# Performance work log

Hardware: AMD Instinct MI355X
Metric: run time of the kernel (lower is better)

## Reference

```python
import jax, jax.numpy as jnp
import numpy as np

N = 100000      # nodes
E = 1600000     # edges
F_IN = 27       # node features
EMB = 64        # embedding size
H = 128         # hidden/out channels
L = 4           # GNN layers
G = 512         # num_graphs


def setup_inputs() -> dict:
    key = jax.random.key(0)
    ks = jax.random.split(key, 13)
    s = 0.05
    return {
        "x": jax.random.normal(ks[0], (N, F_IN), jnp.float32),
        "edge_index": jax.random.randint(ks[1], (2, E), 0, N),
        "batch": jnp.sort(jax.random.randint(ks[2], (N,), 0, G)),
        "lin0_w": jax.random.normal(ks[3], (F_IN, EMB), jnp.float32) * s,
        "ggc_weight": jax.random.normal(ks[4], (L, H, H), jnp.float32) * s,
        "gru_w_ih": jax.random.normal(ks[5], (3 * H, H), jnp.float32) * s,
        "gru_w_hh": jax.random.normal(ks[6], (3 * H, H), jnp.float32) * s,
        "gru_b_ih": jax.random.normal(ks[7], (3 * H,), jnp.float32) * s,
        "gru_b_hh": jax.random.normal(ks[8], (3 * H,), jnp.float32) * s,
        "lin1_w": jax.random.normal(ks[9], (H, 1), jnp.float32) * s,
        "lin1_b": jax.random.normal(ks[10], (1,), jnp.float32) * s,
        "lin2_w": jax.random.normal(ks[11], (H, 1), jnp.float32) * s,
        "lin2_b": jax.random.normal(ks[12], (1,), jnp.float32) * s,
    }


def _gru_cell(m, h, w_ih, w_hh, b_ih, b_hh):
    # torch.nn.GRUCell math
    gi = m @ w_ih.T + b_ih          # [N, 3H]
    gh = h @ w_hh.T + b_hh          # [N, 3H]
    i_r, i_z, i_n = jnp.split(gi, 3, axis=1)
    h_r, h_z, h_n = jnp.split(gh, 3, axis=1)
    r = jax.nn.sigmoid(i_r + h_r)
    z = jax.nn.sigmoid(i_z + h_z)
    n = jnp.tanh(i_n + r * h_n)
    return (1.0 - z) * n + z * h


def reference(x, edge_index, batch, lin0_w, ggc_weight,
              gru_w_ih, gru_w_hh, gru_b_ih, gru_b_hh,
              lin1_w, lin1_b, lin2_w, lin2_b):
    x1 = jax.nn.sigmoid(x @ lin0_w)                       # [N, EMB]
    h = jnp.pad(x1, ((0, 0), (0, H - EMB)))               # pad to out_channels
    src, dst = edge_index[0], edge_index[1]
    for i in range(L):
        m = h @ ggc_weight[i]                             # [N, H]
        m = jax.ops.segment_sum(m[src], dst, num_segments=N)  # add-aggregate at target
        h = _gru_cell(m, h, gru_w_ih, gru_w_hh, gru_b_ih, gru_b_hh)
    xr = jax.nn.relu(h)
    mu = xr @ lin1_w + lin1_b                             # [N, 1]
    sigma = jax.nn.softplus(xr @ lin2_w + lin2_b)         # [N, 1]
    uncorrected_mu = mu
    mu_all = jax.ops.segment_sum(mu, batch, num_segments=G)        # [G, 1]
    sigma_all = jax.ops.segment_sum(sigma, batch, num_segments=G)  # [G, 1]
    # vectorized per-graph correction (original loops over graphs)
    mu_c = mu - mu_all[batch] * (sigma / sigma_all[batch])
    return (mu_c.squeeze(1), x1, sigma.squeeze(1), uncorrected_mu.squeeze(1))
```

## Files before the change

kernel.cpp:

```cpp
#include <hip/hip_runtime.h>
#include <math.h>

#define NN 100000
#define FIN 27
#define EMB 64
#define HH 128
#define LAYERS 4
#define GG 512
#define SCAN_CHUNK 2048
#define SPAN 512
#define SPANSHIFT 9
#define MAXNB 256
#define ECAP 16384
#define LPAD_US 136
#define TM 32

typedef __attribute__((ext_vector_type(8))) short short8;
typedef __attribute__((ext_vector_type(4))) float floatx4;

__device__ __forceinline__ float sigmf(float x) { return 1.0f / (1.0f + __expf(-x)); }
__device__ __forceinline__ float tanhfast(float x) { return 1.0f - 2.0f / (__expf(2.0f * x) + 1.0f); }

__device__ __forceinline__ unsigned short f2bf(float f) {
    unsigned int u = __float_as_uint(f);
    u += 0x7FFFu + ((u >> 16) & 1u);
    return (unsigned short)(u >> 16);
}

__device__ __forceinline__ float bflo(unsigned int v) { return __uint_as_float(v << 16); }
__device__ __forceinline__ float bfhi(unsigned int v) { return __uint_as_float(v & 0xFFFF0000u); }
__device__ __forceinline__ float bfs(unsigned short v) { return __uint_as_float(((unsigned)v) << 16); }

__global__ void lin0_kernel(const float* __restrict__ x, const float* __restrict__ w,
                            float* __restrict__ x1_out, unsigned short* __restrict__ hbf, int n) {
    int wave = (int)((blockIdx.x * blockDim.x + threadIdx.x) >> 6);
    int lane = threadIdx.x & 63;
    if (wave >= n) return;
    const float* xr = x + (size_t)wave * FIN;
    float acc = 0.0f;
#pragma unroll
    for (int k = 0; k < FIN; ++k) acc += xr[k] * w[k * EMB + lane];
    float v = 1.0f / (1.0f + expf(-acc));
    x1_out[(size_t)wave * EMB + lane] = v;
    hbf[(size_t)wave * HH + lane] = f2bf(v);
}

__global__ void bucket_scatter_direct(const int* __restrict__ src, const int* __restrict__ dst,
                                      int* __restrict__ bucket_cnt, unsigned* __restrict__ ebuf,
                                      int e) {
    __shared__ int lh[MAXNB];
    __shared__ int gb[MAXNB];
    int t = threadIdx.x;
    for (int i = t; i < MAXNB; i += 1024) lh[i] = 0;
    __syncthreads();
    int base = blockIdx.x * 16384;
    int lidx[16], sv[16], dv[16];
#pragma unroll
    for (int i = 0; i < 16; ++i) {
        int eid = base + i * 1024 + t;
        if (eid < e) {
            sv[i] = src[eid];
            dv[i] = dst[eid];
            lidx[i] = atomicAdd(&lh[dv[i] >> SPANSHIFT], 1);
        } else lidx[i] = -1;
    }
    __syncthreads();
    for (int i = t; i < MAXNB; i += 1024) {
        int c = lh[i];
        gb[i] = c ? atomicAdd(&bucket_cnt[i], c) : 0;
    }
    __syncthreads();
#pragma unroll
    for (int i = 0; i < 16; ++i) {
        if (lidx[i] >= 0) {
            int b = dv[i] >> SPANSHIFT;
            int pos = gb[b] + lidx[i];
            if (pos < ECAP) {
                unsigned dl = (unsigned)(dv[i] - (b << SPANSHIFT));
                ebuf[(size_t)b * ECAP + pos] = (dl << 17) | (unsigned)sv[i];
            }
        }
    }
}

__global__ void deg_from_buckets(const unsigned* __restrict__ ebuf, const int* __restrict__ bucket_cnt,
                                 int* __restrict__ deg, int n) {
    __shared__ int ld[SPAN];
    int b = blockIdx.x, t = threadIdx.x;
    ld[t] = 0; ld[t + 256] = 0;
    __syncthreads();
    int cnt = bucket_cnt[b];
    if (cnt > ECAP) cnt = ECAP;
    size_t base = (size_t)b * ECAP;
    int nodebase = b << SPANSHIFT;
    for (int j = t; j < cnt; j += 256)
        atomicAdd(&ld[ebuf[base + j] >> 17], 1);
    __syncthreads();
    int i0 = nodebase + t, i1 = nodebase + 256 + t;
    if (i0 < n) deg[i0] = ld[t];
    if (i1 < n) deg[i1] = ld[t + 256];
}

__global__ void scan_partial(const int* __restrict__ deg, int* __restrict__ blocksum, int n) {
    int b = blockIdx.x, t = threadIdx.x;
    int base = b * SCAN_CHUNK + t * 8;
    int s = 0;
#pragma unroll
    for (int i = 0; i < 8; ++i) {
        int idx = base + i;
        if (idx < n) s += deg[idx];
    }
#pragma unroll
    for (int off = 32; off > 0; off >>= 1) s += __shfl_down(s, off, 64);
    __shared__ int ws[4];
    if ((t & 63) == 0) ws[t >> 6] = s;
    __syncthreads();
    if (t == 0) blocksum[b] = ws[0] + ws[1] + ws[2] + ws[3];
}

__global__ void scan_blocksums(const int* __restrict__ blocksum, int* __restrict__ blockoff, int nb) {
    int t = threadIdx.x;
    int own = (t < nb) ? blocksum[t] : 0;
    int v = own;
    for (int off = 1; off < 64; off <<= 1) {
        int u = __shfl_up(v, off, 64);
        if (t >= off) v += u;
    }
    if (t < nb) blockoff[t] = v - own;
}

__global__ void scan_final(const int* __restrict__ deg, const int* __restrict__ blockoff,
                           int* __restrict__ rowptr, int n) {
    int b = blockIdx.x, t = threadIdx.x;
    int base = b * SCAN_CHUNK + t * 8;
    int v[8];
    int s = 0;
#pragma unroll
    for (int i = 0; i < 8; ++i) {
        int idx = base + i;
        v[i] = (idx < n) ? deg[idx] : 0;
        s += v[i];
    }
    __shared__ int ts[256];
    ts[t] = s;
    __syncthreads();
    for (int off = 1; off < 256; off <<= 1) {
        int u = (t >= off) ? ts[t - off] : 0;
        __syncthreads();
        ts[t] += u;
        __syncthreads();
    }
    int run = blockoff[b] + ((t == 0) ? 0 : ts[t - 1]);
#pragma unroll
    for (int i = 0; i < 8; ++i) {
        int idx = base + i;
        if (idx < n) {
            rowptr[idx] = run;
            run += v[i];
        } else if (idx == n) {
            rowptr[n] = run;
        }
    }
}

__global__ void place_kernel(const unsigned* __restrict__ ebuf, const int* __restrict__ bucket_cnt,
                             const int* __restrict__ rowptr, int* __restrict__ col, int n) {
    __shared__ int cur[SPAN];
    int b = blockIdx.x, t = threadIdx.x;
    int nodebase = b << SPANSHIFT;
    int i0 = nodebase + t, i1 = nodebase + 256 + t;
    cur[t] = (i0 < n) ? rowptr[i0] : 0;
    cur[t + 256] = (i1 < n) ? rowptr[i1] : 0;
    __syncthreads();
    int cnt = bucket_cnt[b];
    if (cnt > ECAP) cnt = ECAP;
    size_t base = (size_t)b * ECAP;
    for (int j = t; j < cnt; j += 256) {
        unsigned ed = ebuf[base + j];
        int pos = atomicAdd(&cur[ed >> 17], 1);
        col[pos] = (int)(ed & 0x1FFFFu);
    }
}

__global__ void sort_rows_kernel(const int* __restrict__ rowptr, int* __restrict__ col, int n) {
    int node = (int)((blockIdx.x * blockDim.x + threadIdx.x) >> 6);
    int lane = threadIdx.x & 63;
    if (node >= n) return;
    int r0 = rowptr[node], r1 = rowptr[node + 1];
    int d = r1 - r0;
    if (d <= 1 || d > 64) return;
    int v = (lane < d) ? col[r0 + lane] : 0x7FFFFFFF;
#pragma unroll
    for (int k = 2; k <= 64; k <<= 1) {
#pragma unroll
        for (int j = k >> 1; j > 0; j >>= 1) {
            int u = __shfl_xor(v, j, 64);
            bool dir = (lane & k) == 0;
            bool lower = (lane & j) == 0;
            int mn = min(v, u), mx = max(v, u);
            v = (dir == lower) ? mn : mx;
        }
    }
    if (lane < d) col[r0 + lane] = v;
}

template <int HALF>
__global__ __launch_bounds__(512, 8)
void agg_kernel(const unsigned short* __restrict__ hin, unsigned short* __restrict__ aggout,
                const int* __restrict__ rowptr, const int* __restrict__ col, int n) {
    int node = (int)((blockIdx.x * blockDim.x + threadIdx.x) >> 6);
    int lane = threadIdx.x & 63;
    if (node >= n) return;
    int l16 = lane & 15;
    int lg = lane >> 4;
    const uint4* hin4 = (const uint4*)hin;
    const uint2* hin2 = (const uint2*)hin;
    int r0 = rowptr[node];
    int r1 = rowptr[node + 1];

    if (HALF) {
        float a[4], b[4];
#pragma unroll
        for (int k = 0; k < 4; ++k) { a[k] = 0.0f; b[k] = 0.0f; }
        int j = r0 + lg;
        for (; j + 4 < r1; j += 8) {
            int s0 = col[j], s1 = col[j + 4];
            uint2 v0 = hin2[(size_t)s0 * 32 + l16];
            uint2 v1 = hin2[(size_t)s1 * 32 + l16];
            a[0] += bflo(v0.x); a[1] += bfhi(v0.x);
            a[2] += bflo(v0.y); a[3] += bfhi(v0.y);
            b[0] += bflo(v1.x); b[1] += bfhi(v1.x);
            b[2] += bflo(v1.y); b[3] += bfhi(v1.y);
        }
        for (; j < r1; j += 4) {
            int s = col[j];
            uint2 v = hin2[(size_t)s * 32 + l16];
            a[0] += bflo(v.x); a[1] += bfhi(v.x);
            a[2] += bflo(v.y); a[3] += bfhi(v.y);
        }
#pragma unroll
        for (int k = 0; k < 4; ++k) {
            a[k] += b[k];
            a[k] += __shfl_xor(a[k], 32, 64);
            a[k] += __shfl_xor(a[k], 16, 64);
        }
        if (lg == 0) {
            uint2 o;
            o.x = (unsigned)f2bf(a[0]) | ((unsigned)f2bf(a[1]) << 16);
            o.y = (unsigned)f2bf(a[2]) | ((unsigned)f2bf(a[3]) << 16);
            *(uint2*)(aggout + (size_t)node * HH + l16 * 4) = o;
        }
    } else {
        float a[8], b[8];
#pragma unroll
        for (int k = 0; k < 8; ++k) { a[k] = 0.0f; b[k] = 0.0f; }
        int j = r0 + lg;
        for (; j + 12 < r1; j += 16) {
            int s0 = col[j], s1 = col[j + 4], s2 = col[j + 8], s3 = col[j + 12];
            uint4 v0 = hin4[(size_t)s0 * 16 + l16];
            uint4 v1 = hin4[(size_t)s1 * 16 + l16];
            uint4 v2 = hin4[(size_t)s2 * 16 + l16];
            uint4 v3 = hin4[(size_t)s3 * 16 + l16];
            a[0] += bflo(v0.x); a[1] += bfhi(v0.x);
            a[2] += bflo(v0.y); a[3] += bfhi(v0.y);
            a[4] += bflo(v0.z); a[5] += bfhi(v0.z);
            a[6] += bflo(v0.w); a[7] += bfhi(v0.w);
            b[0] += bflo(v1.x); b[1] += bfhi(v1.x);
            b[2] += bflo(v1.y); b[3] += bfhi(v1.y);
            b[4] += bflo(v1.z); b[5] += bfhi(v1.z);
            b[6] += bflo(v1.w); b[7] += bfhi(v1.w);
            a[0] += bflo(v2.x); a[1] += bfhi(v2.x);
            a[2] += bflo(v2.y); a[3] += bfhi(v2.y);
            a[4] += bflo(v2.z); a[5] += bfhi(v2.z);
            a[6] += bflo(v2.w); a[7] += bfhi(v2.w);
            b[0] += bflo(v3.x); b[1] += bfhi(v3.x);
            b[2] += bflo(v3.y); b[3] += bfhi(v3.y);
            b[4] += bflo(v3.z); b[5] += bfhi(v3.z);
            b[6] += bflo(v3.w); b[7] += bfhi(v3.w);
        }
        for (; j + 4 < r1; j += 8) {
            int s0 = col[j], s1 = col[j + 4];
            uint4 v0 = hin4[(size_t)s0 * 16 + l16];
            uint4 v1 = hin4[(size_t)s1 * 16 + l16];
            a[0] += bflo(v0.x); a[1] += bfhi(v0.x);
            a[2] += bflo(v0.y); a[3] += bfhi(v0.y);
            a[4] += bflo(v0.z); a[5] += bfhi(v0.z);
            a[6] += bflo(v0.w); a[7] += bfhi(v0.w);
            b[0] += bflo(v1.x); b[1] += bfhi(v1.x);
            b[2] += bflo(v1.y); b[3] += bfhi(v1.y);
            b[4] += bflo(v1.z); b[5] += bfhi(v1.z);
            b[6] += bflo(v1.w); b[7] += bfhi(v1.w);
        }
        for (; j < r1; j += 4) {
            int s = col[j];
            uint4 v = hin4[(size_t)s * 16 + l16];
            a[0] += bflo(v.x); a[1] += bfhi(v.x);
            a[2] += bflo(v.y); a[3] += bfhi(v.y);
            a[4] += bflo(v.z); a[5] += bfhi(v.z);
            a[6] += bflo(v.w); a[7] += bfhi(v.w);
        }
#pragma unroll
        for (int k = 0; k < 8; ++k) {
            a[k] += b[k];
            a[k] += __shfl_xor(a[k], 32, 64);
            a[k] += __shfl_xor(a[k], 16, 64);
        }
        if (lg == 0) {
            uint4 o;
            o.x = (unsigned)f2bf(a[0]) | ((unsigned)f2bf(a[1]) << 16);
            o.y = (unsigned)f2bf(a[2]) | ((unsigned)f2bf(a[3]) << 16);
            o.z = (unsigned)f2bf(a[4]) | ((unsigned)f2bf(a[5]) << 16);
            o.w = (unsigned)f2bf(a[6]) | ((unsigned)f2bf(a[7]) << 16);
            *(uint4*)(aggout + (size_t)node * HH + l16 * 8) = o;
        }
    }
}

template <int HALF>
__global__ __launch_bounds__(512, 4)
void gru_kernel(const unsigned short* __restrict__ aggin,
                const unsigned short* __restrict__ hin,
                unsigned short* __restrict__ hout,
                const unsigned short* __restrict__ Wfp,
                const unsigned short* __restrict__ whhp,
                const float* __restrict__ b_ih, const float* __restrict__ b_hh,
                int n) {
    __shared__ unsigned short aggL[TM * LPAD_US];
    __shared__ unsigned short hL[TM * LPAD_US];
    int wave = threadIdx.x >> 6;
    int lane = threadIdx.x & 63;
    int quad = lane >> 4;
    int l15 = lane & 15;
    int M0 = blockIdx.x * TM;
    if (M0 >= n) return;

    {
        int row = threadIdx.x >> 4;
        int q = threadIdx.x & 15;
        int gr = M0 + row;
        uint4 va = make_uint4(0, 0, 0, 0), vh = va;
        if (gr < n && !(HALF && q >= 8)) {
            va = ((const uint4*)aggin)[(size_t)gr * 16 + q];
            vh = ((const uint4*)hin)[(size_t)gr * 16 + q];
        }
        *(uint4*)(&aggL[row * LPAD_US + q * 8]) = va;
        *(uint4*)(&hL[row * LPAD_US + q * 8]) = vh;
    }
    __syncthreads();

    floatx4 gi[2][3], gh[2][3];
#pragma unroll
    for (int m = 0; m < 2; ++m)
#pragma unroll
        for (int g = 0; g < 3; ++g) {
            gi[m][g] = (floatx4)0.0f;
            gh[m][g] = (floatx4)0.0f;
        }

    const int KTMAX = HALF ? 2 : 4;
#pragma unroll
    for (int kt = 0; kt < KTMAX; ++kt) {
        int kbase = kt * 32 + quad * 8;
        short8 aA0 = *(const short8*)(&aggL[l15 * LPAD_US + kbase]);
        short8 aH0 = *(const short8*)(&hL[l15 * LPAD_US + kbase]);
        short8 aA1 = *(const short8*)(&aggL[(16 + l15) * LPAD_US + kbase]);
        short8 aH1 = *(const short8*)(&hL[(16 + l15) * LPAD_US + kbase]);
#pragma unroll
        for (int g = 0; g < 3; ++g) {
            int ct = g * 8 + wave;
            size_t boff = ((size_t)(kt * 24 + ct) * 64 + lane) * 8;
            short8 bi = *(const short8*)(Wfp + boff);
            short8 bh = *(const short8*)(whhp + boff);
            gi[0][g] = __builtin_amdgcn_mfma_f32_16x16x32_bf16(aA0, bi, gi[0][g], 0, 0, 0);
            gi[1][g] = __builtin_amdgcn_mfma_f32_16x16x32_bf16(aA1, bi, gi[1][g], 0, 0, 0);
            gh[0][g] = __builtin_amdgcn_mfma_f32_16x16x32_bf16(aH0, bh, gh[0][g], 0, 0, 0);
            gh[1][g] = __builtin_amdgcn_mfma_f32_16x16x32_bf16(aH1, bh, gh[1][g], 0, 0, 0);
        }
    }

    __syncthreads();

    {
        int c = wave * 16 + l15;
        float bir = b_ih[c], biz = b_ih[128 + c], bin_ = b_ih[256 + c];
        float bhr = b_hh[c], bhz = b_hh[128 + c], bhn = b_hh[256 + c];
#pragma unroll
        for (int m = 0; m < 2; ++m) {
#pragma unroll
            for (int j = 0; j < 4; ++j) {
                int row = m * 16 + quad * 4 + j;
                int lidx = row * LPAD_US + c;
                float gir = gi[m][0][j] + bir;
                float ghr = gh[m][0][j] + bhr;
                float giz = gi[m][1][j] + biz;
                float ghz = gh[m][1][j] + bhz;
                float gin = gi[m][2][j] + bin_;
                float ghn = gh[m][2][j] + bhn;
                float rr = sigmf(gir + ghr);
                float zz = sigmf(giz + ghz);
                float nn = tanhfast(gin + rr * ghn);
                float hp = bfs(hL[lidx]);
                aggL[lidx] = f2bf((1.0f - zz) * nn + zz * hp);
            }
        }
    }

    __syncthreads();

    {
        int row = threadIdx.x >> 4;
        int q = threadIdx.x & 15;
        int gr = M0 + row;
        if (gr < n) {
            uint4 v = *(const uint4*)(&aggL[row * LPAD_US + q * 8]);
            *(uint4*)(hout + (size_t)gr * HH + q * 8) = v;
        }
    }
}

__global__ void pack_whh(const float* __restrict__ w_hh, unsigned short* __restrict__ whhp) {
    int id = blockIdx.x * blockDim.x + threadIdx.x;
    if (id >= 4 * 24 * 64 * 8) return;
    int j = id & 7;
    int lane = (id >> 3) & 63;
    int ctkt = id >> 9;
    int ct = ctkt % 24;
    int kt = ctkt / 24;
    int k = kt * 32 + (lane >> 4) * 8 + j;
    int col = ct * 16 + (lane & 15);
    whhp[id] = f2bf(w_hh[col * HH + k]);
}

__global__ void pack_wf(const float* __restrict__ ggc, const float* __restrict__ w_ih,
                        unsigned short* __restrict__ Wfp) {
    int id = blockIdx.x * blockDim.x + threadIdx.x;
    if (id >= LAYERS * 4 * 24 * 64 * 8) return;
    int l = id / 49152;
    int rem = id % 49152;
    int j = rem & 7;
    int lane = (rem >> 3) & 63;
    int ctkt = rem >> 9;
    int ct = ctkt % 24;
    int kt = ctkt / 24;
    int k = kt * 32 + (lane >> 4) * 8 + j;
    int col = ct * 16 + (lane & 15);
    const float4* gr = (const float4*)(ggc + ((size_t)l * HH + k) * HH);
    const float4* wr = (const float4*)(w_ih + (size_t)col * HH);
    float acc = 0.0f;
#pragma unroll 4
    for (int q = 0; q < HH / 4; ++q) {
        float4 g = gr[q], w = wr[q];
        acc += g.x * w.x + g.y * w.y + g.z * w.z + g.w * w.w;
    }
    Wfp[id] = f2bf(acc);
}

__global__ void readout_kernel(const unsigned int* __restrict__ h2, const float* __restrict__ w1,
                               const float* __restrict__ b1, const float* __restrict__ w2,
                               const float* __restrict__ b2,
                               float* __restrict__ out_mu, float* __restrict__ out_sg, int n) {
    int wave = (int)((blockIdx.x * blockDim.x + threadIdx.x) >> 6);
    int lane = threadIdx.x & 63;
    if (wave >= n) return;
    unsigned int u = h2[(size_t)wave * 64 + lane];
    float x0 = fmaxf(bflo(u), 0.0f);
    float x1 = fmaxf(bfhi(u), 0.0f);
    float2 wv1 = ((const float2*)w1)[lane];
    float2 wv2 = ((const float2*)w2)[lane];
    float a1 = x0 * wv1.x + x1 * wv1.y;
    float a2 = x0 * wv2.x + x1 * wv2.y;
#pragma unroll
    for (int off = 32; off > 0; off >>= 1) {
        a1 += __shfl_down(a1, off, 64);
        a2 += __shfl_down(a2, off, 64);
    }
    if (lane == 0) {
        float mu = a1 + b1[0];
        float x2 = a2 + b2[0];
        float sg = (x2 > 20.0f) ? x2 : __logf(1.0f + __expf(x2));
        out_mu[wave] = mu;
        out_sg[wave] = sg;
    }
}

__device__ __forceinline__ int lbound(const int* __restrict__ a, int n, int v) {
    int lo = 0, hi = n;
    while (lo < hi) {
        int m = (lo + hi) >> 1;
        if (a[m] < v) lo = m + 1; else hi = m;
    }
    return lo;
}

__global__ void seg_correct_kernel(const float* __restrict__ out_mu, const float* __restrict__ out_sg,
                                   const int* __restrict__ batch, float* __restrict__ out_muc, int n) {
    int g = blockIdx.x;
    int lo = lbound(batch, n, g);
    int hi = lbound(batch, n, g + 1);
    float smu = 0.0f, ssg = 0.0f;
    for (int i = lo + threadIdx.x; i < hi; i += blockDim.x) {
        smu += out_mu[i];
        ssg += out_sg[i];
    }
#pragma unroll
    for (int off = 32; off > 0; off >>= 1) {
        smu += __shfl_down(smu, off, 64);
        ssg += __shfl_down(ssg, off, 64);
    }
    __shared__ float pm[4], ps[4];
    int wave = threadIdx.x >> 6;
    int lane = threadIdx.x & 63;
    if (lane == 0) { pm[wave] = smu; ps[wave] = ssg; }
    __syncthreads();
    float tot_mu = pm[0] + pm[1] + pm[2] + pm[3];
    float tot_sg = ps[0] + ps[1] + ps[2] + ps[3];
    for (int i = lo + threadIdx.x; i < hi; i += blockDim.x) {
        out_muc[i] = out_mu[i] - tot_mu * (out_sg[i] / tot_sg);
    }
}

extern "C" void kernel_launch(void* const* d_in, const int* in_sizes, int n_in,
                              void* d_out, int out_size, void* d_ws, size_t ws_size,
                              hipStream_t stream) {
    const float* x      = (const float*)d_in[0];
    const int*   ei     = (const int*)d_in[1];
    const int*   batch  = (const int*)d_in[2];
    const float* lin0_w = (const float*)d_in[3];
    const float* ggc    = (const float*)d_in[4];
    const float* w_ih   = (const float*)d_in[5];
    const float* w_hh   = (const float*)d_in[6];
    const float* b_ih   = (const float*)d_in[7];
    const float* b_hh   = (const float*)d_in[8];
    const float* l1w    = (const float*)d_in[9];
    const float* l1b    = (const float*)d_in[10];
    const float* l2w    = (const float*)d_in[11];
    const float* l2b    = (const float*)d_in[12];

    int n = in_sizes[0] / FIN;
    int e = in_sizes[1] / 2;
    const int* src = ei;
    const int* dstp = ei + e;

    float* out = (float*)d_out;
    float* out_muc = out;
    float* out_x1  = out + n;
    float* out_sg  = out + n + (size_t)n * EMB;
    float* out_mu  = out_sg + n;

    unsigned short* hbf0 = (unsigned short*)d_ws;
    unsigned short* hbf1 = hbf0 + (size_t)n * HH;
    unsigned short* Wfp  = hbf1 + (size_t)n * HH;
    unsigned short* whhp = Wfp + (size_t)LAYERS * 49152;
    int*            deg      = (int*)(whhp + 49152 + 8);
    int*            rowptr   = deg + n;
    int*            blocksum = rowptr + n + 1;
    int*            blockoff = blocksum + 64;
    int*            bucket_cnt = blockoff + 64;
    int*            col      = bucket_cnt + MAXNB;
    unsigned*       ebuf     = (unsigned*)hbf1;

    int nbuck = (n + SPAN - 1) >> SPANSHIFT;
    hipMemsetAsync(bucket_cnt, 0, MAXNB * sizeof(int), stream);

    int wave_blocks = (n * 64 + 255) / 256;
    lin0_kernel<<<wave_blocks, 256, 0, stream>>>(x, lin0_w, out_x1, hbf0, n);

    int eb = (e + 16383) / 16384;
    bucket_scatter_direct<<<eb, 1024, 0, stream>>>(src, dstp, bucket_cnt, ebuf, e);
    deg_from_buckets<<<nbuck, 256, 0, stream>>>(ebuf, bucket_cnt, deg, n);

    int nb = (n + SCAN_CHUNK) / SCAN_CHUNK;
    scan_partial<<<nb, 256, 0, stream>>>(deg, blocksum, n);
    scan_blocksums<<<1, 64, 0, stream>>>(blocksum, blockoff, nb);
    scan_final<<<nb, 256, 0, stream>>>(deg, blockoff, rowptr, n);

    place_kernel<<<nbuck, 256, 0, stream>>>(ebuf, bucket_cnt, rowptr, col, n);

    int node_wave_blocks = (n + 7) / 8;
    sort_rows_kernel<<<node_wave_blocks, 512, 0, stream>>>(rowptr, col, n);

    pack_whh<<<(49152 + 255) / 256, 256, 0, stream>>>(w_hh, whhp);
    pack_wf<<<(LAYERS * 49152 + 255) / 256, 256, 0, stream>>>(ggc, w_ih, Wfp);

    int gru_blocks = (n + TM - 1) / TM;
    unsigned short* hin = hbf0;
    unsigned short* hother = hbf1;
    for (int l = 0; l < LAYERS; ++l) {
        if (l == 0) {
            agg_kernel<1><<<node_wave_blocks, 512, 0, stream>>>(hin, hother, rowptr, col, n);
            gru_kernel<1><<<gru_blocks, 512, 0, stream>>>(hother, hin, hother,
                                                          Wfp, whhp, b_ih, b_hh, n);
        } else {
            agg_kernel<0><<<node_wave_blocks, 512, 0, stream>>>(hin, hother, rowptr, col, n);
            gru_kernel<0><<<gru_blocks, 512, 0, stream>>>(hother, hin, hother,
                                                          Wfp + (size_t)l * 49152, whhp,
                                                          b_ih, b_hh, n);
        }
        unsigned short* t = hin; hin = hother; hother = t;
    }

    readout_kernel<<<wave_blocks, 256, 0, stream>>>((const unsigned int*)hin, l1w, l1b, l2w, l2b,
                                                    out_mu, out_sg, n);
    seg_correct_kernel<<<GG, 256, 0, stream>>>(out_mu, out_sg, batch, out_muc, n);
}
```

Before: 653.8 us.

## Double GRU row tile to 64 and drop per-row neighbor sort kernel

The GRU kernel now processes 64 rows per block instead of 32, so each weight fragment loaded from global memory feeds four MFMA row tiles instead of two. Launch bounds are relaxed to allow more registers for the larger accumulator set. Separately, the bitonic sort of each node's neighbor list is removed, saving a kernel launch, though the order of summation in aggregation then depends on atomic placement and is no longer deterministic. The larger tile raises register and LDS use, which lowers occupancy.

Measured after the change: 667.6 us. 2.1% more time.

```diff
diff --git a/kernel.cpp b/kernel.cpp
--- a/kernel.cpp
+++ b/kernel.cpp
@@ -13,7 +13,7 @@
 #define MAXNB 256
 #define ECAP 16384
 #define LPAD_US 136
-#define TM 32
+#define TM 64
 
 typedef __attribute__((ext_vector_type(8))) short short8;
 typedef __attribute__((ext_vector_type(4))) float floatx4;
@@ -180,28 +180,6 @@
         int pos = atomicAdd(&cur[ed >> 17], 1);
         col[pos] = (int)(ed & 0x1FFFFu);
     }
-}
-
-__global__ void sort_rows_kernel(const int* __restrict__ rowptr, int* __restrict__ col, int n) {
-    int node = (int)((blockIdx.x * blockDim.x + threadIdx.x) >> 6);
-    int lane = threadIdx.x & 63;
-    if (node >= n) return;
-    int r0 = rowptr[node], r1 = rowptr[node + 1];
-    int d = r1 - r0;
-    if (d <= 1 || d > 64) return;
-    int v = (lane < d) ? col[r0 + lane] : 0x7FFFFFFF;
-#pragma unroll
-    for (int k = 2; k <= 64; k <<= 1) {
-#pragma unroll
-        for (int j = k >> 1; j > 0; j >>= 1) {
-            int u = __shfl_xor(v, j, 64);
-            bool dir = (lane & k) == 0;
-            bool lower = (lane & j) == 0;
-            int mn = min(v, u), mx = max(v, u);
-            v = (dir == lower) ? mn : mx;
-        }
-    }
-    if (lane < d) col[r0 + lane] = v;
 }
 
 template <int HALF>
@@ -317,7 +295,7 @@
 }
 
 template <int HALF>
-__global__ __launch_bounds__(512, 4)
+__global__ __launch_bounds__(512, 2)
 void gru_kernel(const unsigned short* __restrict__ aggin,
                 const unsigned short* __restrict__ hin,
                 unsigned short* __restrict__ hout,
@@ -334,9 +312,11 @@
     int M0 = blockIdx.x * TM;
     if (M0 >= n) return;
 
-    {
-        int row = threadIdx.x >> 4;
-        int q = threadIdx.x & 15;
+#pragma unroll
+    for (int i = 0; i < 2; ++i) {
+        int idx = threadIdx.x + i * 512;
+        int row = idx >> 4;
+        int q = idx & 15;
         int gr = M0 + row;
         uint4 va = make_uint4(0, 0, 0, 0), vh = va;
         if (gr < n && !(HALF && q >= 8)) {
@@ -348,9 +328,9 @@
     }
     __syncthreads();
 
-    floatx4 gi[2][3], gh[2][3];
-#pragma unroll
-    for (int m = 0; m < 2; ++m)
+    floatx4 gi[4][3], gh[4][3];
+#pragma unroll
+    for (int m = 0; m < 4; ++m)
 #pragma unroll
         for (int g = 0; g < 3; ++g) {
             gi[m][g] = (floatx4)0.0f;
@@ -361,20 +341,23 @@
 #pragma unroll
     for (int kt = 0; kt < KTMAX; ++kt) {
         int kbase = kt * 32 + quad * 8;
-        short8 aA0 = *(const short8*)(&aggL[l15 * LPAD_US + kbase]);
-        short8 aH0 = *(const short8*)(&hL[l15 * LPAD_US + kbase]);
-        short8 aA1 = *(const short8*)(&aggL[(16 + l15) * LPAD_US + kbase]);
-        short8 aH1 = *(const short8*)(&hL[(16 + l15) * LPAD_US + kbase]);
+        short8 aA[4], aH[4];
+#pragma unroll
+        for (int m = 0; m < 4; ++m) {
+            aA[m] = *(const short8*)(&aggL[(m * 16 + l15) * LPAD_US + kbase]);
+            aH[m] = *(const short8*)(&hL[(m * 16 + l15) * LPAD_US + kbase]);
+        }
 #pragma unroll
         for (int g = 0; g < 3; ++g) {
             int ct = g * 8 + wave;
             size_t boff = ((size_t)(kt * 24 + ct) * 64 + lane) * 8;
             short8 bi = *(const short8*)(Wfp + boff);
             short8 bh = *(const short8*)(whhp + boff);
-            gi[0][g] = __builtin_amdgcn_mfma_f32_16x16x32_bf16(aA0, bi, gi[0][g], 0, 0, 0);
-            gi[1][g] = __builtin_amdgcn_mfma_f32_16x16x32_bf16(aA1, bi, gi[1][g], 0, 0, 0);
-            gh[0][g] = __builtin_amdgcn_mfma_f32_16x16x32_bf16(aH0, bh, gh[0][g], 0, 0, 0);
-            gh[1][g] = __builtin_amdgcn_mfma_f32_16x16x32_bf16(aH1, bh, gh[1][g], 0, 0, 0);
+#pragma unroll
+            for (int m = 0; m < 4; ++m) {
+                gi[m][g] = __builtin_amdgcn_mfma_f32_16x16x32_bf16(aA[m], bi, gi[m][g], 0, 0, 0);
+                gh[m][g] = __builtin_amdgcn_mfma_f32_16x16x32_bf16(aH[m], bh, gh[m][g], 0, 0, 0);
+            }
         }
     }
 
@@ -385,7 +368,7 @@
         float bir = b_ih[c], biz = b_ih[128 + c], bin_ = b_ih[256 + c];
         float bhr = b_hh[c], bhz = b_hh[128 + c], bhn = b_hh[256 + c];
 #pragma unroll
-        for (int m = 0; m < 2; ++m) {
+        for (int m = 0; m < 4; ++m) {
 #pragma unroll
             for (int j = 0; j < 4; ++j) {
                 int row = m * 16 + quad * 4 + j;
@@ -407,9 +390,11 @@
 
     __syncthreads();
 
-    {
-        int row = threadIdx.x >> 4;
-        int q = threadIdx.x & 15;
+#pragma unroll
+    for (int i = 0; i < 2; ++i) {
+        int idx = threadIdx.x + i * 512;
+        int row = idx >> 4;
+        int q = idx & 15;
         int gr = M0 + row;
         if (gr < n) {
             uint4 v = *(const uint4*)(&aggL[row * LPAD_US + q * 8]);
@@ -576,12 +561,10 @@
 
     place_kernel<<<nbuck, 256, 0, stream>>>(ebuf, bucket_cnt, rowptr, col, n);
 
-    int node_wave_blocks = (n + 7) / 8;
-    sort_rows_kernel<<<node_wave_blocks, 512, 0, stream>>>(rowptr, col, n);
-
     pack_whh<<<(49152 + 255) / 256, 256, 0, stream>>>(w_hh, whhp);
     pack_wf<<<(LAYERS * 49152 + 255) / 256, 256, 0, stream>>>(ggc, w_ih, Wfp);
 
+    int node_wave_blocks = (n + 7) / 8;
     int gru_blocks = (n + TM - 1) / TM;
     unsigned short* hin = hbf0;
     unsigned short* hother = hbf1;
```

## Merge aggregation and GRU into chunked launches and drop row sorting

Applied to the files above, without the earlier changes.

Each layer is split into node chunks. One launch runs the GRU update for chunk k-1 alongside the neighbor aggregation for chunk k, so the gather and matrix phases overlap instead of being separated by kernel boundaries. The per-row column sort kernel is removed, which saves a pass but leaves gather order within rows unsorted and may hurt locality. The change adds more launches per layer and a mixed-role block dispatch that can unbalance occupancy.

New measurement: 808.4 us. 1.24x slower.

```diff
diff --git a/kernel.cpp b/kernel.cpp
--- a/kernel.cpp
+++ b/kernel.cpp
@@ -13,7 +13,8 @@
 #define MAXNB 256
 #define ECAP 16384
 #define LPAD_US 136
-#define TM 32
+#define TMG 32
+#define KCH 4
 
 typedef __attribute__((ext_vector_type(8))) short short8;
 typedef __attribute__((ext_vector_type(4))) float floatx4;
@@ -182,238 +183,212 @@
     }
 }
 
-__global__ void sort_rows_kernel(const int* __restrict__ rowptr, int* __restrict__ col, int n) {
-    int node = (int)((blockIdx.x * blockDim.x + threadIdx.x) >> 6);
-    int lane = threadIdx.x & 63;
-    if (node >= n) return;
-    int r0 = rowptr[node], r1 = rowptr[node + 1];
-    int d = r1 - r0;
-    if (d <= 1 || d > 64) return;
-    int v = (lane < d) ? col[r0 + lane] : 0x7FFFFFFF;
-#pragma unroll
-    for (int k = 2; k <= 64; k <<= 1) {
-#pragma unroll
-        for (int j = k >> 1; j > 0; j >>= 1) {
-            int u = __shfl_xor(v, j, 64);
-            bool dir = (lane & k) == 0;
-            bool lower = (lane & j) == 0;
-            int mn = min(v, u), mx = max(v, u);
-            v = (dir == lower) ? mn : mx;
-        }
-    }
-    if (lane < d) col[r0 + lane] = v;
-}
-
-template <int HALF>
-__global__ __launch_bounds__(512, 8)
-void agg_kernel(const unsigned short* __restrict__ hin, unsigned short* __restrict__ aggout,
-                const int* __restrict__ rowptr, const int* __restrict__ col, int n) {
-    int node = (int)((blockIdx.x * blockDim.x + threadIdx.x) >> 6);
-    int lane = threadIdx.x & 63;
-    if (node >= n) return;
-    int l16 = lane & 15;
-    int lg = lane >> 4;
-    const uint4* hin4 = (const uint4*)hin;
-    const uint2* hin2 = (const uint2*)hin;
-    int r0 = rowptr[node];
-    int r1 = rowptr[node + 1];
-
-    if (HALF) {
-        float a[4], b[4];
-#pragma unroll
-        for (int k = 0; k < 4; ++k) { a[k] = 0.0f; b[k] = 0.0f; }
-        int j = r0 + lg;
-        for (; j + 4 < r1; j += 8) {
-            int s0 = col[j], s1 = col[j + 4];
-            uint2 v0 = hin2[(size_t)s0 * 32 + l16];
-            uint2 v1 = hin2[(size_t)s1 * 32 + l16];
-            a[0] += bflo(v0.x); a[1] += bfhi(v0.x);
-            a[2] += bflo(v0.y); a[3] += bfhi(v0.y);
-            b[0] += bflo(v1.x); b[1] += bfhi(v1.x);
-            b[2] += bflo(v1.y); b[3] += bfhi(v1.y);
-        }
-        for (; j < r1; j += 4) {
-            int s = col[j];
-            uint2 v = hin2[(size_t)s * 32 + l16];
-            a[0] += bflo(v.x); a[1] += bfhi(v.x);
-            a[2] += bflo(v.y); a[3] += bfhi(v.y);
-        }
-#pragma unroll
-        for (int k = 0; k < 4; ++k) {
-            a[k] += b[k];
-            a[k] += __shfl_xor(a[k], 32, 64);
-            a[k] += __shfl_xor(a[k], 16, 64);
-        }
-        if (lg == 0) {
-            uint2 o;
-            o.x = (unsigned)f2bf(a[0]) | ((unsigned)f2bf(a[1]) << 16);
-            o.y = (unsigned)f2bf(a[2]) | ((unsigned)f2bf(a[3]) << 16);
-            *(uint2*)(aggout + (size_t)node * HH + l16 * 4) = o;
-        }
-    } else {
-        float a[8], b[8];
-#pragma unroll
-        for (int k = 0; k < 8; ++k) { a[k] = 0.0f; b[k] = 0.0f; }
-        int j = r0 + lg;
-        for (; j + 12 < r1; j += 16) {
-            int s0 = col[j], s1 = col[j + 4], s2 = col[j + 8], s3 = col[j + 12];
-            uint4 v0 = hin4[(size_t)s0 * 16 + l16];
-            uint4 v1 = hin4[(size_t)s1 * 16 + l16];
-            uint4 v2 = hin4[(size_t)s2 * 16 + l16];
-            uint4 v3 = hin4[(size_t)s3 * 16 + l16];
-            a[0] += bflo(v0.x); a[1] += bfhi(v0.x);
-            a[2] += bflo(v0.y); a[3] += bfhi(v0.y);
-            a[4] += bflo(v0.z); a[5] += bfhi(v0.z);
-            a[6] += bflo(v0.w); a[7] += bfhi(v0.w);
-            b[0] += bflo(v1.x); b[1] += bfhi(v1.x);
-            b[2] += bflo(v1.y); b[3] += bfhi(v1.y);
-            b[4] += bflo(v1.z); b[5] += bfhi(v1.z);
-            b[6] += bflo(v1.w); b[7] += bfhi(v1.w);
-            a[0] += bflo(v2.x); a[1] += bfhi(v2.x);
-            a[2] += bflo(v2.y); a[3] += bfhi(v2.y);
-            a[4] += bflo(v2.z); a[5] += bfhi(v2.z);
-            a[6] += bflo(v2.w); a[7] += bfhi(v2.w);
-            b[0] += bflo(v3.x); b[1] += bfhi(v3.x);
-            b[2] += bflo(v3.y); b[3] += bfhi(v3.y);
-            b[4] += bflo(v3.z); b[5] += bfhi(v3.z);
-            b[6] += bflo(v3.w); b[7] += bfhi(v3.w);
-        }
-        for (; j + 4 < r1; j += 8) {
-            int s0 = col[j], s1 = col[j + 4];
-            uint4 v0 = hin4[(size_t)s0 * 16 + l16];
-            uint4 v1 = hin4[(size_t)s1 * 16 + l16];
-            a[0] += bflo(v0.x); a[1] += bfhi(v0.x);
-            a[2] += bflo(v0.y); a[3] += bfhi(v0.y);
-            a[4] += bflo(v0.z); a[5] += bfhi(v0.z);
-            a[6] += bflo(v0.w); a[7] += bfhi(v0.w);
-            b[0] += bflo(v1.x); b[1] += bfhi(v1.x);
-            b[2] += bflo(v1.y); b[3] += bfhi(v1.y);
-            b[4] += bflo(v1.z); b[5] += bfhi(v1.z);
-            b[6] += bflo(v1.w); b[7] += bfhi(v1.w);
-        }
-        for (; j < r1; j += 4) {
-            int s = col[j];
-            uint4 v = hin4[(size_t)s * 16 + l16];
-            a[0] += bflo(v.x); a[1] += bfhi(v.x);
-            a[2] += bflo(v.y); a[3] += bfhi(v.y);
-            a[4] += bflo(v.z); a[5] += bfhi(v.z);
-            a[6] += bflo(v.w); a[7] += bfhi(v.w);
-        }
-#pragma unroll
-        for (int k = 0; k < 8; ++k) {
-            a[k] += b[k];
-            a[k] += __shfl_xor(a[k], 32, 64);
-            a[k] += __shfl_xor(a[k], 16, 64);
-        }
-        if (lg == 0) {
-            uint4 o;
-            o.x = (unsigned)f2bf(a[0]) | ((unsigned)f2bf(a[1]) << 16);
-            o.y = (unsigned)f2bf(a[2]) | ((unsigned)f2bf(a[3]) << 16);
-            o.z = (unsigned)f2bf(a[4]) | ((unsigned)f2bf(a[5]) << 16);
-            o.w = (unsigned)f2bf(a[6]) | ((unsigned)f2bf(a[7]) << 16);
-            *(uint4*)(aggout + (size_t)node * HH + l16 * 8) = o;
-        }
-    }
-}
-
 template <int HALF>
 __global__ __launch_bounds__(512, 4)
-void gru_kernel(const unsigned short* __restrict__ aggin,
-                const unsigned short* __restrict__ hin,
-                unsigned short* __restrict__ hout,
-                const unsigned short* __restrict__ Wfp,
-                const unsigned short* __restrict__ whhp,
-                const float* __restrict__ b_ih, const float* __restrict__ b_hh,
-                int n) {
-    __shared__ unsigned short aggL[TM * LPAD_US];
-    __shared__ unsigned short hL[TM * LPAD_US];
-    int wave = threadIdx.x >> 6;
-    int lane = threadIdx.x & 63;
-    int quad = lane >> 4;
-    int l15 = lane & 15;
-    int M0 = blockIdx.x * TM;
-    if (M0 >= n) return;
-
-    {
-        int row = threadIdx.x >> 4;
-        int q = threadIdx.x & 15;
-        int gr = M0 + row;
-        uint4 va = make_uint4(0, 0, 0, 0), vh = va;
-        if (gr < n && !(HALF && q >= 8)) {
-            va = ((const uint4*)aggin)[(size_t)gr * 16 + q];
-            vh = ((const uint4*)hin)[(size_t)gr * 16 + q];
-        }
-        *(uint4*)(&aggL[row * LPAD_US + q * 8]) = va;
-        *(uint4*)(&hL[row * LPAD_US + q * 8]) = vh;
-    }
-    __syncthreads();
-
-    floatx4 gi[2][3], gh[2][3];
-#pragma unroll
-    for (int m = 0; m < 2; ++m)
-#pragma unroll
-        for (int g = 0; g < 3; ++g) {
-            gi[m][g] = (floatx4)0.0f;
-            gh[m][g] = (floatx4)0.0f;
-        }
-
-    const int KTMAX = HALF ? 2 : 4;
-#pragma unroll
-    for (int kt = 0; kt < KTMAX; ++kt) {
-        int kbase = kt * 32 + quad * 8;
-        short8 aA0 = *(const short8*)(&aggL[l15 * LPAD_US + kbase]);
-        short8 aH0 = *(const short8*)(&hL[l15 * LPAD_US + kbase]);
-        short8 aA1 = *(const short8*)(&aggL[(16 + l15) * LPAD_US + kbase]);
-        short8 aH1 = *(const short8*)(&hL[(16 + l15) * LPAD_US + kbase]);
-#pragma unroll
-        for (int g = 0; g < 3; ++g) {
-            int ct = g * 8 + wave;
-            size_t boff = ((size_t)(kt * 24 + ct) * 64 + lane) * 8;
-            short8 bi = *(const short8*)(Wfp + boff);
-            short8 bh = *(const short8*)(whhp + boff);
-            gi[0][g] = __builtin_amdgcn_mfma_f32_16x16x32_bf16(aA0, bi, gi[0][g], 0, 0, 0);
-            gi[1][g] = __builtin_amdgcn_mfma_f32_16x16x32_bf16(aA1, bi, gi[1][g], 0, 0, 0);
-            gh[0][g] = __builtin_amdgcn_mfma_f32_16x16x32_bf16(aH0, bh, gh[0][g], 0, 0, 0);
-            gh[1][g] = __builtin_amdgcn_mfma_f32_16x16x32_bf16(aH1, bh, gh[1][g], 0, 0, 0);
-        }
-    }
-
-    __syncthreads();
-
-    {
-        int c = wave * 16 + l15;
-        float bir = b_ih[c], biz = b_ih[128 + c], bin_ = b_ih[256 + c];
-        float bhr = b_hh[c], bhz = b_hh[128 + c], bhn = b_hh[256 + c];
-#pragma unroll
-        for (int m = 0; m < 2; ++m) {
-#pragma unroll
-            for (int j = 0; j < 4; ++j) {
-                int row = m * 16 + quad * 4 + j;
-                int lidx = row * LPAD_US + c;
-                float gir = gi[m][0][j] + bir;
-                float ghr = gh[m][0][j] + bhr;
-                float giz = gi[m][1][j] + biz;
-                float ghz = gh[m][1][j] + bhz;
-                float gin = gi[m][2][j] + bin_;
-                float ghn = gh[m][2][j] + bhn;
-                float rr = sigmf(gir + ghr);
-                float zz = sigmf(giz + ghz);
-                float nn = tanhfast(gin + rr * ghn);
-                float hp = bfs(hL[lidx]);
-                aggL[lidx] = f2bf((1.0f - zz) * nn + zz * hp);
-            }
-        }
-    }
-
-    __syncthreads();
-
-    {
-        int row = threadIdx.x >> 4;
-        int q = threadIdx.x & 15;
-        int gr = M0 + row;
-        if (gr < n) {
-            uint4 v = *(const uint4*)(&aggL[row * LPAD_US + q * 8]);
-            *(uint4*)(hout + (size_t)gr * HH + q * 8) = v;
+void layer_chunk(const unsigned short* __restrict__ hin,
+                 unsigned short* __restrict__ bufA,
+                 const int* __restrict__ rowptr, const int* __restrict__ col,
+                 const unsigned short* __restrict__ Wfp,
+                 const unsigned short* __restrict__ whhp,
+                 const float* __restrict__ b_ih, const float* __restrict__ b_hh,
+                 int aggLo, int aggHi, int gruLo, int gruHi, int gruBlocks) {
+    __shared__ unsigned short aggL[TMG * LPAD_US];
+    __shared__ unsigned short hL[TMG * LPAD_US];
+
+    if ((int)blockIdx.x < gruBlocks) {
+        int wave = threadIdx.x >> 6;
+        int lane = threadIdx.x & 63;
+        int quad = lane >> 4;
+        int l15 = lane & 15;
+        int M0 = gruLo + (int)blockIdx.x * TMG;
+
+        {
+            int row = threadIdx.x >> 4;
+            int q = threadIdx.x & 15;
+            int gr = M0 + row;
+            uint4 va = make_uint4(0, 0, 0, 0), vh = va;
+            if (gr < gruHi && !(HALF && q >= 8)) {
+                va = ((const uint4*)bufA)[(size_t)gr * 16 + q];
+                vh = ((const uint4*)hin)[(size_t)gr * 16 + q];
+            }
+            *(uint4*)(&aggL[row * LPAD_US + q * 8]) = va;
+            *(uint4*)(&hL[row * LPAD_US + q * 8]) = vh;
+        }
+        __syncthreads();
+
+        floatx4 gi[2][3], gh[2][3];
+#pragma unroll
+        for (int m = 0; m < 2; ++m)
+#pragma unroll
+            for (int g = 0; g < 3; ++g) {
+                gi[m][g] = (floatx4)0.0f;
+                gh[m][g] = (floatx4)0.0f;
+            }
+
+        const int KTMAX = HALF ? 2 : 4;
+#pragma unroll
+        for (int kt = 0; kt < KTMAX; ++kt) {
+            int kbase = kt * 32 + quad * 8;
+            short8 aA0 = *(const short8*)(&aggL[l15 * LPAD_US + kbase]);
+            short8 aH0 = *(const short8*)(&hL[l15 * LPAD_US + kbase]);
+            short8 aA1 = *(const short8*)(&aggL[(16 + l15) * LPAD_US + kbase]);
+            short8 aH1 = *(const short8*)(&hL[(16 + l15) * LPAD_US + kbase]);
+#pragma unroll
+            for (int g = 0; g < 3; ++g) {
+                int ct = g * 8 + wave;
+                size_t boff = ((size_t)(kt * 24 + ct) * 64 + lane) * 8;
+                short8 bi = *(const short8*)(Wfp + boff);
+                short8 bh = *(const short8*)(whhp + boff);
+                gi[0][g] = __builtin_amdgcn_mfma_f32_16x16x32_bf16(aA0, bi, gi[0][g], 0, 0, 0);
+                gi[1][g] = __builtin_amdgcn_mfma_f32_16x16x32_bf16(aA1, bi, gi[1][g], 0, 0, 0);
+                gh[0][g] = __builtin_amdgcn_mfma_f32_16x16x32_bf16(aH0, bh, gh[0][g], 0, 0, 0);
+                gh[1][g] = __builtin_amdgcn_mfma_f32_16x16x32_bf16(aH1, bh, gh[1][g], 0, 0, 0);
+            }
+        }
+
+        __syncthreads();
+
+        {
+            int c = wave * 16 + l15;
+            float bir = b_ih[c], biz = b_ih[128 + c], bin_ = b_ih[256 + c];
+            float bhr = b_hh[c], bhz = b_hh[128 + c], bhn = b_hh[256 + c];
+#pragma unroll
+            for (int m = 0; m < 2; ++m) {
+#pragma unroll
+                for (int j = 0; j < 4; ++j) {
+                    int row = m * 16 + quad * 4 + j;
+                    int lidx = row * LPAD_US + c;
+                    float gir = gi[m][0][j] + bir;
+                    float ghr = gh[m][0][j] + bhr;
+                    float giz = gi[m][1][j] + biz;
+                    float ghz = gh[m][1][j] + bhz;
+                    float gin = gi[m][2][j] + bin_;
+                    float ghn = gh[m][2][j] + bhn;
+                    float rr = sigmf(gir + ghr);
+                    float zz = sigmf(giz + ghz);
+                    float nn = tanhfast(gin + rr * ghn);
+                    float hp = bfs(hL[lidx]);
+                    aggL[lidx] = f2bf((1.0f - zz) * nn + zz * hp);
+                }
+            }
+        }
+        __syncthreads();
+
+        {
+            int row = threadIdx.x >> 4;
+            int q = threadIdx.x & 15;
+            int gr = M0 + row;
+            if (gr < gruHi) {
+                uint4 v = *(const uint4*)(&aggL[row * LPAD_US + q * 8]);
+                *(uint4*)(bufA + (size_t)gr * HH + q * 8) = v;
+            }
+        }
+    } else {
+        int node = aggLo + ((int)blockIdx.x - gruBlocks) * 8 + (threadIdx.x >> 6);
+        int lane = threadIdx.x & 63;
+        if (node >= aggHi) return;
+        int l16 = lane & 15;
+        int lg = lane >> 4;
+        const uint4* hin4 = (const uint4*)hin;
+        const uint2* hin2 = (const uint2*)hin;
+        int r0 = rowptr[node];
+        int r1 = rowptr[node + 1];
+
+        if (HALF) {
+            float a[4], b[4];
+#pragma unroll
+            for (int k = 0; k < 4; ++k) { a[k] = 0.0f; b[k] = 0.0f; }
+            int j = r0 + lg;
+            for (; j + 4 < r1; j += 8) {
+                int s0 = col[j], s1 = col[j + 4];
+                uint2 v0 = hin2[(size_t)s0 * 32 + l16];
+                uint2 v1 = hin2[(size_t)s1 * 32 + l16];
+                a[0] += bflo(v0.x); a[1] += bfhi(v0.x);
+                a[2] += bflo(v0.y); a[3] += bfhi(v0.y);
+                b[0] += bflo(v1.x); b[1] += bfhi(v1.x);
+                b[2] += bflo(v1.y); b[3] += bfhi(v1.y);
+            }
+            for (; j < r1; j += 4) {
+                int s = col[j];
+                uint2 v = hin2[(size_t)s * 32 + l16];
+                a[0] += bflo(v.x); a[1] += bfhi(v.x);
+                a[2] += bflo(v.y); a[3] += bfhi(v.y);
+            }
+#pragma unroll
+            for (int k = 0; k < 4; ++k) {
+                a[k] += b[k];
+                a[k] += __shfl_xor(a[k], 32, 64);
+                a[k] += __shfl_xor(a[k], 16, 64);
+            }
+            if (lg == 0) {
+                uint2 o;
+                o.x = (unsigned)f2bf(a[0]) | ((unsigned)f2bf(a[1]) << 16);
+                o.y = (unsigned)f2bf(a[2]) | ((unsigned)f2bf(a[3]) << 16);
+                *(uint2*)(bufA + (size_t)node * HH + l16 * 4) = o;
+            }
+        } else {
+            float a[8], b[8];
+#pragma unroll
+            for (int k = 0; k < 8; ++k) { a[k] = 0.0f; b[k] = 0.0f; }
+            int j = r0 + lg;
+            for (; j + 12 < r1; j += 16) {
+                int s0 = col[j], s1 = col[j + 4], s2 = col[j + 8], s3 = col[j + 12];
+                uint4 v0 = hin4[(size_t)s0 * 16 + l16];
+                uint4 v1 = hin4[(size_t)s1 * 16 + l16];
+                uint4 v2 = hin4[(size_t)s2 * 16 + l16];
+                uint4 v3 = hin4[(size_t)s3 * 16 + l16];
+                a[0] += bflo(v0.x); a[1] += bfhi(v0.x);
+                a[2] += bflo(v0.y); a[3] += bfhi(v0.y);
+                a[4] += bflo(v0.z); a[5] += bfhi(v0.z);
+                a[6] += bflo(v0.w); a[7] += bfhi(v0.w);
+                b[0] += bflo(v1.x); b[1] += bfhi(v1.x);
+                b[2] += bflo(v1.y); b[3] += bfhi(v1.y);
+                b[4] += bflo(v1.z); b[5] += bfhi(v1.z);
+                b[6] += bflo(v1.w); b[7] += bfhi(v1.w);
+                a[0] += bflo(v2.x); a[1] += bfhi(v2.x);
+                a[2] += bflo(v2.y); a[3] += bfhi(v2.y);
+                a[4] += bflo(v2.z); a[5] += bfhi(v2.z);
+                a[6] += bflo(v2.w); a[7] += bfhi(v2.w);
+                b[0] += bflo(v3.x); b[1] += bfhi(v3.x);
+                b[2] += bflo(v3.y); b[3] += bfhi(v3.y);
+                b[4] += bflo(v3.z); b[5] += bfhi(v3.z);
+                b[6] += bflo(v3.w); b[7] += bfhi(v3.w);
+            }
+            for (; j + 4 < r1; j += 8) {
+                int s0 = col[j], s1 = col[j + 4];
+                uint4 v0 = hin4[(size_t)s0 * 16 + l16];
+                uint4 v1 = hin4[(size_t)s1 * 16 + l16];
+                a[0] += bflo(v0.x); a[1] += bfhi(v0.x);
+                a[2] += bflo(v0.y); a[3] += bfhi(v0.y);
+                a[4] += bflo(v0.z); a[5] += bfhi(v0.z);
+                a[6] += bflo(v0.w); a[7] += bfhi(v0.w);
+                b[0] += bflo(v1.x); b[1] += bfhi(v1.x);
+                b[2] += bflo(v1.y); b[3] += bfhi(v1.y);
+                b[4] += bflo(v1.z); b[5] += bfhi(v1.z);
+                b[6] += bflo(v1.w); b[7] += bfhi(v1.w);
+            }
+            for (; j < r1; j += 4) {
+                int s = col[j];
+                uint4 v = hin4[(size_t)s * 16 + l16];
+                a[0] += bflo(v.x); a[1] += bfhi(v.x);
+                a[2] += bflo(v.y); a[3] += bfhi(v.y);
+                a[4] += bflo(v.z); a[5] += bfhi(v.z);
+                a[6] += bflo(v.w); a[7] += bfhi(v.w);
+            }
+#pragma unroll
+            for (int k = 0; k < 8; ++k) {
+                a[k] += b[k];
+                a[k] += __shfl_xor(a[k], 32, 64);
+                a[k] += __shfl_xor(a[k], 16, 64);
+            }
+            if (lg == 0) {
+                uint4 o;
+                o.x = (unsigned)f2bf(a[0]) | ((unsigned)f2bf(a[1]) << 16);
+                o.y = (unsigned)f2bf(a[2]) | ((unsigned)f2bf(a[3]) << 16);
+                o.z = (unsigned)f2bf(a[4]) | ((unsigned)f2bf(a[5]) << 16);
+                o.w = (unsigned)f2bf(a[6]) | ((unsigned)f2bf(a[7]) << 16);
+                *(uint4*)(bufA + (size_t)node * HH + l16 * 8) = o;
+            }
         }
     }
 }
@@ -576,25 +551,31 @@
 
     place_kernel<<<nbuck, 256, 0, stream>>>(ebuf, bucket_cnt, rowptr, col, n);
 
-    int node_wave_blocks = (n + 7) / 8;
-    sort_rows_kernel<<<node_wave_blocks, 512, 0, stream>>>(rowptr, col, n);
-
     pack_whh<<<(49152 + 255) / 256, 256, 0, stream>>>(w_hh, whhp);
     pack_wf<<<(LAYERS * 49152 + 255) / 256, 256, 0, stream>>>(ggc, w_ih, Wfp);
 
-    int gru_blocks = (n + TM - 1) / TM;
+    int cs = (n + KCH - 1) / KCH;
     unsigned short* hin = hbf0;
     unsigned short* hother = hbf1;
     for (int l = 0; l < LAYERS; ++l) {
-        if (l == 0) {
-            agg_kernel<1><<<node_wave_blocks, 512, 0, stream>>>(hin, hother, rowptr, col, n);
-            gru_kernel<1><<<gru_blocks, 512, 0, stream>>>(hother, hin, hother,
-                                                          Wfp, whhp, b_ih, b_hh, n);
-        } else {
-            agg_kernel<0><<<node_wave_blocks, 512, 0, stream>>>(hin, hother, rowptr, col, n);
-            gru_kernel<0><<<gru_blocks, 512, 0, stream>>>(hother, hin, hother,
-                                                          Wfp + (size_t)l * 49152, whhp,
-                                                          b_ih, b_hh, n);
+        const unsigned short* Wl = Wfp + (size_t)l * 49152;
+        for (int k = 0; k <= KCH; ++k) {
+            int aLo = (k < KCH) ? k * cs : 0;
+            int aHi = (k < KCH) ? ((k + 1) * cs < n ? (k + 1) * cs : n) : 0;
+            int gLo = (k >= 1) ? (k - 1) * cs : 0;
+            int gHi = (k >= 1) ? (k * cs < n ? k * cs : n) : 0;
+            int aggB = (aHi > aLo) ? (aHi - aLo + 7) / 8 : 0;
+            int gruB = (gHi > gLo) ? (gHi - gLo + TMG - 1) / TMG : 0;
+            if (aggB + gruB == 0) continue;
+            if (l == 0) {
+                layer_chunk<1><<<aggB + gruB, 512, 0, stream>>>(
+                    hin, hother, rowptr, col, Wl, whhp, b_ih, b_hh,
+                    aLo, aHi, gLo, gHi, gruB);
+            } else {
+                layer_chunk<0><<<aggB + gruB, 512, 0, stream>>>(
+                    hin, hother, rowptr, col, Wl, whhp, b_ih, b_hh,
+                    aLo, aHi, gLo, gHi, gruB);
+            }
         }
         unsigned short* t = hin; hin = hother; hother = t;
     }
```
